# Kernel optimization log

Measured on AMD Instinct MI355X. Metric: run time of the kernel, lower is better.

Reference implementation:

```python
import jax, jax.numpy as jnp
import numpy as np


def setup_inputs() -> dict:
    key = jax.random.key(0)
    k1, k2, k3 = jax.random.split(key, 3)
    B, N, D, F = 4, 4096, 128, 128
    features = jax.random.normal(k1, (B, N, D), dtype=jnp.float32)
    A = jax.random.uniform(k2, (B, N, N), dtype=jnp.float32)
    weight = jax.random.normal(k3, (D, F), dtype=jnp.float32) * (6.0 / (D + F)) ** 0.5
    bias = jnp.zeros((F,), dtype=jnp.float32)
    return {"features": features, "A": A, "weight": weight, "bias": bias}


def reference(features, A, weight, bias):
    # aggregate: per-batch adjacency matmul  [B,N,N] @ [B,N,D] -> [B,N,D]
    agg = jnp.einsum("bnm,bmd->bnd", A, features)
    # linear transform + bias + relu  [B,N,D] @ [D,F] -> [B,N,F]
    out = jnp.einsum("bnd,df->bnf", agg, weight) + bias
    return jax.nn.relu(out)
```

## Files before the change

### kernel.cpp

```cpp
#include <hip/hip_runtime.h>
#include <hip/hip_bf16.h>

typedef __attribute__((ext_vector_type(4))) float  float4v;
typedef __attribute__((ext_vector_type(4))) short  short4v;
typedef __attribute__((ext_vector_type(8))) short  short8v;
typedef __attribute__((ext_vector_type(4))) float  f32x4;

__device__ __forceinline__ short f2bf(float f) {
  __hip_bfloat16 h = __float2bfloat16(f);
  return *reinterpret_cast<short*>(&h);
}

__device__ __forceinline__ short8v cvt8(float4v v0, float4v v1) {
  short8v s;
  s[0]=f2bf(v0[0]); s[1]=f2bf(v0[1]); s[2]=f2bf(v0[2]); s[3]=f2bf(v0[3]);
  s[4]=f2bf(v1[0]); s[5]=f2bf(v1[1]); s[6]=f2bf(v1[2]); s[7]=f2bf(v1[3]);
  return s;
}

__device__ __forceinline__ int swz(int row, int k, int ld) {
  return row * ld + (k ^ ((row & 7) << 3));
}

__device__ __forceinline__ void gll16(const void* g, void* l) {
  __builtin_amdgcn_global_load_lds(
      (const __attribute__((address_space(1))) unsigned int*)g,
      (__attribute__((address_space(3))) unsigned int*)l, 16, 0, 0);
}

__global__ __launch_bounds__(256) void k0_wt(const float* __restrict__ W,
                                             short* __restrict__ wt) {
  const int task = blockIdx.x * 256 + threadIdx.x;
  const int f = task & 127;
  const int dc = (task >> 7) * 8;
  short8v s;
#pragma unroll
  for (int j = 0; j < 8; ++j) s[j] = f2bf(W[(size_t)(dc + j) * 128 + f]);
  *(short8v*)(wt + (size_t)f * 128 + dc) = s;
}

__global__ __launch_bounds__(256) void k1_feat_x_w(
    const float* __restrict__ feat, const short* __restrict__ wt,
    short* __restrict__ ht, int N) {
  const int t = threadIdx.x;
  const int batch = blockIdx.y;
  const int m0 = blockIdx.x * 64;
  const int lane = t & 63, wid = t >> 6;
  const int lr = lane & 15, lk = (lane >> 4) * 8;
  const float* pa = feat + (size_t)batch * N * 128
                  + (size_t)(m0 + wid * 16 + lr) * 128 + lk;

  f32x4 acc[8];
#pragma unroll
  for (int j = 0; j < 8; ++j) acc[j] = (f32x4){0.f, 0.f, 0.f, 0.f};

#pragma unroll
  for (int kk = 0; kk < 4; ++kk) {
    float4v v0 = ((const float4v*)(pa + kk * 32))[0];
    float4v v1 = ((const float4v*)(pa + kk * 32))[1];
    short8v a = cvt8(v0, v1);
#pragma unroll
    for (int ni = 0; ni < 8; ++ni) {
      short8v b = *(const short8v*)(wt + (size_t)(ni * 16 + lr) * 128 + kk * 32 + lk);
      acc[ni] = __builtin_amdgcn_mfma_f32_16x16x32_bf16(a, b, acc[ni], 0, 0, 0);
    }
  }

  short* hb = ht + (size_t)batch * 128 * N;
  const int m = m0 + wid * 16 + (lane >> 4) * 4;
#pragma unroll
  for (int ni = 0; ni < 8; ++ni) {
    const int f = ni * 16 + lr;
    short4v s;
#pragma unroll
    for (int r = 0; r < 4; ++r) s[r] = f2bf(acc[ni][r]);
    *(short4v*)(hb + (size_t)f * N + m) = s;
  }
}

__global__ __launch_bounds__(256, 4) void k2_a_x_h(
    const float* __restrict__ A, const short* __restrict__ ht,
    const float* __restrict__ bias, float* __restrict__ out, int N) {
  __shared__ __align__(16) short As[2][16 * 64];
  __shared__ __align__(16) short Hs[2][128 * 64];
  const int t = threadIdx.x;

  const int nwg = gridDim.x * gridDim.y;
  int wg = blockIdx.x + gridDim.x * blockIdx.y;
  wg = (wg & 7) * (nwg >> 3) + (wg >> 3);
  const int mtiles = gridDim.x;
  const int batch = wg / mtiles;
  const int m0 = (wg - batch * mtiles) * 16;

  const float* Ab = A + (size_t)batch * N * N;
  const short* hb = ht + (size_t)batch * 128 * N;

  const int lane = t & 63, wid = t >> 6;
  const int lr = lane & 15, lk = (lane >> 4) * 8;

  const int arow = t >> 4;
  const int akc = (t & 15) * 4;

  const int hf = lane >> 3;
  const int hks = (lane & 7) * 8;

  float4v va;
  auto loadA = [&](int k0) {
    va = *(const float4v*)(Ab + (size_t)(m0 + arow) * N + k0 + akc);
  };
  auto writeA = [&](int buf) {
    short4v s;
#pragma unroll
    for (int i = 0; i < 4; ++i) s[i] = f2bf(va[i]);
    *(short4v*)(&As[buf][swz(arow, akc, 64)]) = s;
  };
  auto stageH = [&](int k0, int buf) {
#pragma unroll
    for (int i = 0; i < 4; ++i) {
      const int fb8 = (wid * 4 + i) * 8;
      const int f = fb8 + hf;
      const short* g = hb + (size_t)f * N + k0 + (hks ^ (hf << 3));
      gll16(g, &Hs[buf][fb8 * 64]);
    }
  };

  f32x4 acc[2];
  acc[0] = (f32x4){0.f, 0.f, 0.f, 0.f};
  acc[1] = (f32x4){0.f, 0.f, 0.f, 0.f};

  loadA(0);
  stageH(0, 0);
  writeA(0);
  __syncthreads();

  const int NT = N / 64;
  for (int tt = 0; tt < NT; ++tt) {
    const int cur = tt & 1;
    const bool pf = (tt + 1 < NT);
    if (pf) {
      loadA((tt + 1) * 64);
      stageH((tt + 1) * 64, cur ^ 1);
    }
#pragma unroll
    for (int kk = 0; kk < 2; ++kk) {
      const int k = kk * 32 + lk;
      short8v a = *(const short8v*)(&As[cur][swz(lr, k, 64)]);
#pragma unroll
      for (int ni = 0; ni < 2; ++ni) {
        short8v b = *(const short8v*)(&Hs[cur][swz(wid * 32 + ni * 16 + lr, k, 64)]);
        acc[ni] = __builtin_amdgcn_mfma_f32_16x16x32_bf16(a, b, acc[ni], 0, 0, 0);
      }
    }
    if (pf) writeA(cur ^ 1);
    __syncthreads();
  }

  float* ob = out + (size_t)batch * N * 128;
#pragma unroll
  for (int ni = 0; ni < 2; ++ni) {
    const int f = wid * 32 + ni * 16 + lr;
    const float bv = bias[f];
    const int mbase = m0 + (lane >> 4) * 4;
#pragma unroll
    for (int r = 0; r < 4; ++r)
      ob[(size_t)(mbase + r) * 128 + f] = fmaxf(acc[ni][r] + bv, 0.f);
  }
}

extern "C" void kernel_launch(void* const* d_in, const int* in_sizes, int n_in,
                              void* d_out, int out_size, void* d_ws, size_t ws_size,
                              hipStream_t stream) {
  const float* feat = (const float*)d_in[0];
  const float* A    = (const float*)d_in[1];
  const float* W    = (const float*)d_in[2];
  const float* bias = (const float*)d_in[3];
  float* out = (float*)d_out;

  const int featN = in_sizes[0];
  const int aN    = in_sizes[1];
  const int BN    = featN / 128;
  const int N     = aN / BN;
  const int Bb    = BN / N;

  short* wt = (short*)d_ws;
  short* ht = wt + 128 * 128;

  dim3 blk(256);
  hipLaunchKernelGGL(k0_wt, dim3(8), blk, 0, stream, W, wt);
  hipLaunchKernelGGL(k1_feat_x_w, dim3(N / 64, Bb), blk, 0, stream, feat, wt, ht, N);
  hipLaunchKernelGGL(k2_a_x_h, dim3(N / 16, Bb), blk, 0, stream, A, ht, bias, out, N);
}
```

Baseline: 93.03 us.

## Stream A directly into registers with per-wave double-buffered H and 32-row tiles

Restructures the A×H kernel so each 128-thread block handles 32 output rows. Each wave owns 64 output features and its own LDS slice of H. A is loaded straight into registers and converted to bf16 just before the MFMAs, so A no longer goes through LDS. Double buffering now uses explicit vmcnt waits instead of __syncthreads. The larger M tile halves the H re-read per output row, at the cost of far fewer waves per CU and more registers per thread.

```diff
diff --git a/kernel.cpp b/kernel.cpp
--- a/kernel.cpp
+++ b/kernel.cpp
@@ -27,6 +27,9 @@
       (const __attribute__((address_space(1))) unsigned int*)g,
       (__attribute__((address_space(3))) unsigned int*)l, 16, 0, 0);
 }
+
+#define SB() __builtin_amdgcn_sched_barrier(0)
+#define WAIT16() asm volatile("s_waitcnt vmcnt(16)" ::: "memory")
 
 __global__ __launch_bounds__(256) void k0_wt(const float* __restrict__ W,
                                              short* __restrict__ wt) {
@@ -78,92 +81,97 @@
   }
 }
 
-__global__ __launch_bounds__(256, 4) void k2_a_x_h(
+__global__ __launch_bounds__(128, 1) void k2_a_x_h(
     const float* __restrict__ A, const short* __restrict__ ht,
     const float* __restrict__ bias, float* __restrict__ out, int N) {
-  __shared__ __align__(16) short As[2][16 * 64];
-  __shared__ __align__(16) short Hs[2][128 * 64];
+  __shared__ __align__(16) short Hs[2][2][64 * 64];
   const int t = threadIdx.x;
+  const int lane = t & 63, fh = t >> 6;
 
   const int nwg = gridDim.x * gridDim.y;
   int wg = blockIdx.x + gridDim.x * blockIdx.y;
-  wg = (wg & 7) * (nwg >> 3) + (wg >> 3);
+  if ((nwg & 7) == 0) wg = (wg & 7) * (nwg >> 3) + (wg >> 3);
   const int mtiles = gridDim.x;
   const int batch = wg / mtiles;
-  const int m0 = (wg - batch * mtiles) * 16;
+  const int m0 = (wg - batch * mtiles) * 32;
 
   const float* Ab = A + (size_t)batch * N * N;
-  const short* hb = ht + (size_t)batch * 128 * N;
+  const short* hb = ht + (size_t)batch * 128 * N + (size_t)fh * 64 * N;
 
-  const int lane = t & 63, wid = t >> 6;
   const int lr = lane & 15, lk = (lane >> 4) * 8;
+  const int hf = lane >> 3, hks = (lane & 7) * 8;
 
-  const int arow = t >> 4;
-  const int akc = (t & 15) * 4;
+  short* H0 = &Hs[fh][0][0];
+  short* H1 = &Hs[fh][1][0];
 
-  const int hf = lane >> 3;
-  const int hks = (lane & 7) * 8;
-
-  float4v va;
-  auto loadA = [&](int k0) {
-    va = *(const float4v*)(Ab + (size_t)(m0 + arow) * N + k0 + akc);
-  };
-  auto writeA = [&](int buf) {
-    short4v s;
+  auto stageH = [&](int k0, short* dst) {
 #pragma unroll
-    for (int i = 0; i < 4; ++i) s[i] = f2bf(va[i]);
-    *(short4v*)(&As[buf][swz(arow, akc, 64)]) = s;
-  };
-  auto stageH = [&](int k0, int buf) {
-#pragma unroll
-    for (int i = 0; i < 4; ++i) {
-      const int fb8 = (wid * 4 + i) * 8;
-      const int f = fb8 + hf;
-      const short* g = hb + (size_t)f * N + k0 + (hks ^ (hf << 3));
-      gll16(g, &Hs[buf][fb8 * 64]);
+    for (int i = 0; i < 8; ++i) {
+      const int f8 = i * 8;
+      const short* g = hb + (size_t)(f8 + hf) * N + k0 + (hks ^ (hf << 3));
+      gll16(g, dst + f8 * 64);
     }
   };
+  auto loadA = [&](int k0, float4v (&ar)[8]) {
+    const float* p0 = Ab + (size_t)(m0 + lr) * N + k0 + lk;
+    const float* p1 = p0 + (size_t)16 * N;
+    ar[0] = ((const float4v*)p0)[0];          ar[1] = ((const float4v*)p0)[1];
+    ar[2] = ((const float4v*)(p0 + 32))[0];   ar[3] = ((const float4v*)(p0 + 32))[1];
+    ar[4] = ((const float4v*)p1)[0];          ar[5] = ((const float4v*)p1)[1];
+    ar[6] = ((const float4v*)(p1 + 32))[0];   ar[7] = ((const float4v*)(p1 + 32))[1];
+  };
 
-  f32x4 acc[2];
-  acc[0] = (f32x4){0.f, 0.f, 0.f, 0.f};
-  acc[1] = (f32x4){0.f, 0.f, 0.f, 0.f};
+  f32x4 acc[2][4];
+#pragma unroll
+  for (int i = 0; i < 2; ++i)
+#pragma unroll
+    for (int j = 0; j < 4; ++j) acc[i][j] = (f32x4){0.f, 0.f, 0.f, 0.f};
 
-  loadA(0);
-  stageH(0, 0);
-  writeA(0);
-  __syncthreads();
+  auto compute = [&](const short* Hbuf, float4v (&ar)[8]) {
+    short8v a[2][2];
+    a[0][0] = cvt8(ar[0], ar[1]);  a[0][1] = cvt8(ar[2], ar[3]);
+    a[1][0] = cvt8(ar[4], ar[5]);  a[1][1] = cvt8(ar[6], ar[7]);
+#pragma unroll
+    for (int kk = 0; kk < 2; ++kk)
+#pragma unroll
+      for (int ni = 0; ni < 4; ++ni) {
+        short8v b = *(const short8v*)(Hbuf + swz(ni * 16 + lr, kk * 32 + lk, 64));
+#pragma unroll
+        for (int mi = 0; mi < 2; ++mi)
+          acc[mi][ni] = __builtin_amdgcn_mfma_f32_16x16x32_bf16(a[mi][kk], b, acc[mi][ni], 0, 0, 0);
+      }
+  };
 
+  float4v arA[8], arB[8];
   const int NT = N / 64;
-  for (int tt = 0; tt < NT; ++tt) {
-    const int cur = tt & 1;
-    const bool pf = (tt + 1 < NT);
-    if (pf) {
-      loadA((tt + 1) * 64);
-      stageH((tt + 1) * 64, cur ^ 1);
-    }
-#pragma unroll
-    for (int kk = 0; kk < 2; ++kk) {
-      const int k = kk * 32 + lk;
-      short8v a = *(const short8v*)(&As[cur][swz(lr, k, 64)]);
-#pragma unroll
-      for (int ni = 0; ni < 2; ++ni) {
-        short8v b = *(const short8v*)(&Hs[cur][swz(wid * 32 + ni * 16 + lr, k, 64)]);
-        acc[ni] = __builtin_amdgcn_mfma_f32_16x16x32_bf16(a, b, acc[ni], 0, 0, 0);
-      }
-    }
-    if (pf) writeA(cur ^ 1);
-    __syncthreads();
+
+  stageH(0, H0);
+  loadA(0, arA);
+  for (int tt = 0; tt < NT; tt += 2) {
+    const int kn = (tt + 1) * 64;
+    stageH(kn, H1);
+    loadA(kn, arB);
+    SB(); WAIT16(); SB();
+    compute(H0, arA);
+    const int kn2 = (tt + 2 < NT) ? (tt + 2) * 64 : (NT - 1) * 64;
+    stageH(kn2, H0);
+    loadA(kn2, arA);
+    SB(); WAIT16(); SB();
+    compute(H1, arB);
   }
 
-  float* ob = out + (size_t)batch * N * 128;
+  float* ob = out + (size_t)batch * N * 128 + fh * 64;
 #pragma unroll
-  for (int ni = 0; ni < 2; ++ni) {
-    const int f = wid * 32 + ni * 16 + lr;
-    const float bv = bias[f];
-    const int mbase = m0 + (lane >> 4) * 4;
+  for (int ni = 0; ni < 4; ++ni) {
+    const int fl = ni * 16 + lr;
+    const float bv = bias[fh * 64 + fl];
 #pragma unroll
-    for (int r = 0; r < 4; ++r)
-      ob[(size_t)(mbase + r) * 128 + f] = fmaxf(acc[ni][r] + bv, 0.f);
+    for (int mi = 0; mi < 2; ++mi) {
+      const int mbase = m0 + mi * 16 + (lane >> 4) * 4;
+#pragma unroll
+      for (int r = 0; r < 4; ++r)
+        ob[(size_t)(mbase + r) * 128 + fl] = fmaxf(acc[mi][ni][r] + bv, 0.f);
+    }
   }
 }
 
@@ -185,8 +193,7 @@
   short* wt = (short*)d_ws;
   short* ht = wt + 128 * 128;
 
-  dim3 blk(256);
-  hipLaunchKernelGGL(k0_wt, dim3(8), blk, 0, stream, W, wt);
-  hipLaunchKernelGGL(k1_feat_x_w, dim3(N / 64, Bb), blk, 0, stream, feat, wt, ht, N);
-  hipLaunchKernelGGL(k2_a_x_h, dim3(N / 16, Bb), blk, 0, stream, A, ht, bias, out, N);
+  hipLaunchKernelGGL(k0_wt, dim3(8), dim3(256), 0, stream, W, wt);
+  hipLaunchKernelGGL(k1_feat_x_w, dim3(N / 64, Bb), dim3(256), 0, stream, feat, wt, ht, N);
+  hipLaunchKernelGGL(k2_a_x_h, dim3(N / 32, Bb), dim3(128), 0, stream, A, ht, bias, out, N);
 }
```

Result: slower. 105.7 us (+13.6%).

## Enlarge k2 row tile to 64 with direct-register A loads and triple-buffered H

Applied to the files above, without the earlier changes.

The A×H kernel now gives each block 64 output rows instead of 16. Each wave holds a 16x128 accumulator and loads its A fragment straight from global memory into registers, with no LDS staging. The H tile is triple-buffered through global_load_lds, and the pipeline uses explicit vmcnt waits with one barrier per step, so each H tile is reused by four times as many rows. The cost is a grid four times smaller (1024 blocks), higher register pressure and reliance on hand-tuned vmcnt counts that assume a particular load ordering.

```diff
diff --git a/kernel.cpp b/kernel.cpp
--- a/kernel.cpp
+++ b/kernel.cpp
@@ -78,89 +78,94 @@
   }
 }
 
-__global__ __launch_bounds__(256, 4) void k2_a_x_h(
+__global__ __launch_bounds__(256, 1) void k2_a_x_h(
     const float* __restrict__ A, const short* __restrict__ ht,
     const float* __restrict__ bias, float* __restrict__ out, int N) {
-  __shared__ __align__(16) short As[2][16 * 64];
-  __shared__ __align__(16) short Hs[2][128 * 64];
+  __shared__ __align__(16) short Hs[3][128 * 64];
   const int t = threadIdx.x;
+  const int lane = t & 63, wid = t >> 6;
 
   const int nwg = gridDim.x * gridDim.y;
   int wg = blockIdx.x + gridDim.x * blockIdx.y;
-  wg = (wg & 7) * (nwg >> 3) + (wg >> 3);
+  if ((nwg & 7) == 0) wg = (wg & 7) * (nwg >> 3) + (wg >> 3);
   const int mtiles = gridDim.x;
   const int batch = wg / mtiles;
-  const int m0 = (wg - batch * mtiles) * 16;
+  const int m0 = (wg - batch * mtiles) * 64;
 
   const float* Ab = A + (size_t)batch * N * N;
   const short* hb = ht + (size_t)batch * 128 * N;
 
-  const int lane = t & 63, wid = t >> 6;
   const int lr = lane & 15, lk = (lane >> 4) * 8;
+  const int hf = lane >> 3, hks = (lane & 7) * 8;
 
-  const int arow = t >> 4;
-  const int akc = (t & 15) * 4;
+  const float* pa = Ab + (size_t)(m0 + wid * 16 + lr) * N + lk;
 
-  const int hf = lane >> 3;
-  const int hks = (lane & 7) * 8;
-
-  float4v va;
-  auto loadA = [&](int k0) {
-    va = *(const float4v*)(Ab + (size_t)(m0 + arow) * N + k0 + akc);
-  };
-  auto writeA = [&](int buf) {
-    short4v s;
-#pragma unroll
-    for (int i = 0; i < 4; ++i) s[i] = f2bf(va[i]);
-    *(short4v*)(&As[buf][swz(arow, akc, 64)]) = s;
-  };
-  auto stageH = [&](int k0, int buf) {
+  auto stageH = [&](int k0, short* dst) {
 #pragma unroll
     for (int i = 0; i < 4; ++i) {
-      const int fb8 = (wid * 4 + i) * 8;
-      const int f = fb8 + hf;
-      const short* g = hb + (size_t)f * N + k0 + (hks ^ (hf << 3));
-      gll16(g, &Hs[buf][fb8 * 64]);
+      const int f8 = (wid * 4 + i) * 8;
+      const short* g = hb + (size_t)(f8 + hf) * N + k0 + (hks ^ (hf << 3));
+      gll16(g, dst + f8 * 64);
+    }
+  };
+  auto loadA = [&](int k0, float4v (&ar)[4]) {
+    const float* p = pa + k0;
+    ar[0] = ((const float4v*)p)[0];
+    ar[1] = ((const float4v*)p)[1];
+    ar[2] = ((const float4v*)(p + 32))[0];
+    ar[3] = ((const float4v*)(p + 32))[1];
+  };
+
+  f32x4 acc[8];
+#pragma unroll
+  for (int j = 0; j < 8; ++j) acc[j] = (f32x4){0.f, 0.f, 0.f, 0.f};
+
+  auto compute = [&](const short* Hbuf, float4v (&ar)[4]) {
+    short8v a0 = cvt8(ar[0], ar[1]);
+    short8v a1 = cvt8(ar[2], ar[3]);
+#pragma unroll
+    for (int ni = 0; ni < 8; ++ni) {
+      short8v b = *(const short8v*)(Hbuf + swz(ni * 16 + lr, lk, 64));
+      acc[ni] = __builtin_amdgcn_mfma_f32_16x16x32_bf16(a0, b, acc[ni], 0, 0, 0);
+    }
+#pragma unroll
+    for (int ni = 0; ni < 8; ++ni) {
+      short8v b = *(const short8v*)(Hbuf + swz(ni * 16 + lr, 32 + lk, 64));
+      acc[ni] = __builtin_amdgcn_mfma_f32_16x16x32_bf16(a1, b, acc[ni], 0, 0, 0);
     }
   };
 
-  f32x4 acc[2];
-  acc[0] = (f32x4){0.f, 0.f, 0.f, 0.f};
-  acc[1] = (f32x4){0.f, 0.f, 0.f, 0.f};
+  float4v arE[4], arO[4];
+  const int NT = N / 64;
 
-  loadA(0);
-  stageH(0, 0);
-  writeA(0);
-  __syncthreads();
+  stageH(0, &Hs[0][0]);
+  loadA(0, arE);
+  stageH(64, &Hs[1][0]);
+  loadA(64, arO);
 
-  const int NT = N / 64;
-  for (int tt = 0; tt < NT; ++tt) {
-    const int cur = tt & 1;
-    const bool pf = (tt + 1 < NT);
-    if (pf) {
-      loadA((tt + 1) * 64);
-      stageH((tt + 1) * 64, cur ^ 1);
-    }
-#pragma unroll
-    for (int kk = 0; kk < 2; ++kk) {
-      const int k = kk * 32 + lk;
-      short8v a = *(const short8v*)(&As[cur][swz(lr, k, 64)]);
-#pragma unroll
-      for (int ni = 0; ni < 2; ++ni) {
-        short8v b = *(const short8v*)(&Hs[cur][swz(wid * 32 + ni * 16 + lr, k, 64)]);
-        acc[ni] = __builtin_amdgcn_mfma_f32_16x16x32_bf16(a, b, acc[ni], 0, 0, 0);
-      }
-    }
-    if (pf) writeA(cur ^ 1);
-    __syncthreads();
+#define K2_BODY(T_, AR_)                                                     \
+  {                                                                          \
+    const int t_ = (T_);                                                     \
+    if (t_ == NT - 1) { asm volatile("s_waitcnt vmcnt(4)" ::: "memory"); }   \
+    else              { asm volatile("s_waitcnt vmcnt(12)" ::: "memory"); }  \
+    __builtin_amdgcn_s_barrier();                                            \
+    if (t_ + 2 < NT) stageH((t_ + 2) * 64, &Hs[(t_ + 2) % 3][0]);            \
+    compute(&Hs[t_ % 3][0], AR_);                                            \
+    if (t_ + 2 < NT) loadA((t_ + 2) * 64, AR_);                              \
   }
+
+  for (int tt = 0; tt < NT; tt += 2) {
+    K2_BODY(tt, arE);
+    K2_BODY(tt + 1, arO);
+  }
+#undef K2_BODY
 
   float* ob = out + (size_t)batch * N * 128;
 #pragma unroll
-  for (int ni = 0; ni < 2; ++ni) {
-    const int f = wid * 32 + ni * 16 + lr;
+  for (int ni = 0; ni < 8; ++ni) {
+    const int f = ni * 16 + lr;
     const float bv = bias[f];
-    const int mbase = m0 + (lane >> 4) * 4;
+    const int mbase = m0 + wid * 16 + (lane >> 4) * 4;
 #pragma unroll
     for (int r = 0; r < 4; ++r)
       ob[(size_t)(mbase + r) * 128 + f] = fmaxf(acc[ni][r] + bv, 0.f);
@@ -185,8 +190,7 @@
   short* wt = (short*)d_ws;
   short* ht = wt + 128 * 128;
 
-  dim3 blk(256);
-  hipLaunchKernelGGL(k0_wt, dim3(8), blk, 0, stream, W, wt);
-  hipLaunchKernelGGL(k1_feat_x_w, dim3(N / 64, Bb), blk, 0, stream, feat, wt, ht, N);
-  hipLaunchKernelGGL(k2_a_x_h, dim3(N / 16, Bb), blk, 0, stream, A, ht, bias, out, N);
+  hipLaunchKernelGGL(k0_wt, dim3(8), dim3(256), 0, stream, W, wt);
+  hipLaunchKernelGGL(k1_feat_x_w, dim3(N / 64, Bb), dim3(256), 0, stream, feat, wt, ht, N);
+  hipLaunchKernelGGL(k2_a_x_h, dim3(N / 64, Bb), dim3(256), 0, stream, A, ht, bias, out, N);
 }
```

Measured after the change: 91.68 us. Within noise of the previous version (-1.4%).

## Split-K the adjacency GEMM with 32-row tiles and stage H transpose through LDS

Applied to the files above, without the earlier changes.

The A×H kernel now uses 32-row M tiles, so each staged H tile is reused across twice as many rows. It can optionally split K in two, writing fp32 partials that a new combine kernel sums before adding bias and ReLU. The feat×W kernel now transposes its output through shared memory so global stores are coalesced 16-byte rows. Split-K keeps the grid size constant despite larger tiles, but it adds an extra partials write and read of B*N*128 floats twice, plus another launch, and needs a larger workspace.

```diff
diff --git a/kernel.cpp b/kernel.cpp
--- a/kernel.cpp
+++ b/kernel.cpp
@@ -42,6 +42,7 @@
 __global__ __launch_bounds__(256) void k1_feat_x_w(
     const float* __restrict__ feat, const short* __restrict__ wt,
     short* __restrict__ ht, int N) {
+  __shared__ short T[128][72];
   const int t = threadIdx.x;
   const int batch = blockIdx.y;
   const int m0 = blockIdx.x * 64;
@@ -66,22 +67,32 @@
     }
   }
 
+  const int mloc = wid * 16 + (lane >> 4) * 4;
+#pragma unroll
+  for (int ni = 0; ni < 8; ++ni) {
+    short4v s;
+#pragma unroll
+    for (int r = 0; r < 4; ++r) s[r] = f2bf(acc[ni][r]);
+    *(short4v*)(&T[ni * 16 + lr][mloc]) = s;
+  }
+  __syncthreads();
+
   short* hb = ht + (size_t)batch * 128 * N;
-  const int m = m0 + wid * 16 + (lane >> 4) * 4;
-#pragma unroll
-  for (int ni = 0; ni < 8; ++ni) {
-    const int f = ni * 16 + lr;
-    short4v s;
-#pragma unroll
-    for (int r = 0; r < 4; ++r) s[r] = f2bf(acc[ni][r]);
-    *(short4v*)(hb + (size_t)f * N + m) = s;
-  }
-}
-
+#pragma unroll
+  for (int it = 0; it < 4; ++it) {
+    const int idx = it * 256 + t;
+    const int f = idx >> 3;
+    const int mc = (idx & 7) * 8;
+    short8v v = *(const short8v*)(&T[f][mc]);
+    *(short8v*)(hb + (size_t)f * N + m0 + mc) = v;
+  }
+}
+
+template<int NSPLIT>
 __global__ __launch_bounds__(256, 4) void k2_a_x_h(
     const float* __restrict__ A, const short* __restrict__ ht,
-    const float* __restrict__ bias, float* __restrict__ out, int N) {
-  __shared__ __align__(16) short As[2][16 * 64];
+    const float* __restrict__ bias, float* __restrict__ dst, int N) {
+  __shared__ __align__(16) short As[2][32 * 64];
   __shared__ __align__(16) short Hs[2][128 * 64];
   const int t = threadIdx.x;
 
@@ -89,30 +100,33 @@
   int wg = blockIdx.x + gridDim.x * blockIdx.y;
   wg = (wg & 7) * (nwg >> 3) + (wg >> 3);
   const int mtiles = gridDim.x;
-  const int batch = wg / mtiles;
-  const int m0 = (wg - batch * mtiles) * 16;
+  const int combo = wg / mtiles;
+  const int kh = (NSPLIT == 2) ? (combo & 1) : 0;
+  const int batch = (NSPLIT == 2) ? (combo >> 1) : combo;
+  const int m0 = (wg - combo * mtiles) * 32;
+  const int kbase = kh * (N / NSPLIT);
 
   const float* Ab = A + (size_t)batch * N * N;
   const short* hb = ht + (size_t)batch * 128 * N;
 
   const int lane = t & 63, wid = t >> 6;
+  const int mi = wid >> 1, fj = wid & 1;
   const int lr = lane & 15, lk = (lane >> 4) * 8;
 
-  const int arow = t >> 4;
-  const int akc = (t & 15) * 4;
+  const int arow = t >> 3;
+  const int akc = (t & 7) * 8;
 
   const int hf = lane >> 3;
   const int hks = (lane & 7) * 8;
 
-  float4v va;
+  float4v va0, va1;
   auto loadA = [&](int k0) {
-    va = *(const float4v*)(Ab + (size_t)(m0 + arow) * N + k0 + akc);
+    const float* p = Ab + (size_t)(m0 + arow) * N + k0 + akc;
+    va0 = ((const float4v*)p)[0];
+    va1 = ((const float4v*)p)[1];
   };
   auto writeA = [&](int buf) {
-    short4v s;
-#pragma unroll
-    for (int i = 0; i < 4; ++i) s[i] = f2bf(va[i]);
-    *(short4v*)(&As[buf][swz(arow, akc, 64)]) = s;
+    *(short8v*)(&As[buf][swz(arow, akc, 64)]) = cvt8(va0, va1);
   };
   auto stageH = [&](int k0, int buf) {
 #pragma unroll
@@ -124,30 +138,30 @@
     }
   };
 
-  f32x4 acc[2];
-  acc[0] = (f32x4){0.f, 0.f, 0.f, 0.f};
-  acc[1] = (f32x4){0.f, 0.f, 0.f, 0.f};
-
-  loadA(0);
-  stageH(0, 0);
+  f32x4 acc[4];
+#pragma unroll
+  for (int j = 0; j < 4; ++j) acc[j] = (f32x4){0.f, 0.f, 0.f, 0.f};
+
+  loadA(kbase);
+  stageH(kbase, 0);
   writeA(0);
   __syncthreads();
 
-  const int NT = N / 64;
+  const int NT = (N / NSPLIT) / 64;
   for (int tt = 0; tt < NT; ++tt) {
     const int cur = tt & 1;
     const bool pf = (tt + 1 < NT);
     if (pf) {
-      loadA((tt + 1) * 64);
-      stageH((tt + 1) * 64, cur ^ 1);
+      loadA(kbase + (tt + 1) * 64);
+      stageH(kbase + (tt + 1) * 64, cur ^ 1);
     }
 #pragma unroll
     for (int kk = 0; kk < 2; ++kk) {
       const int k = kk * 32 + lk;
-      short8v a = *(const short8v*)(&As[cur][swz(lr, k, 64)]);
-#pragma unroll
-      for (int ni = 0; ni < 2; ++ni) {
-        short8v b = *(const short8v*)(&Hs[cur][swz(wid * 32 + ni * 16 + lr, k, 64)]);
+      short8v a = *(const short8v*)(&As[cur][swz(mi * 16 + lr, k, 64)]);
+#pragma unroll
+      for (int ni = 0; ni < 4; ++ni) {
+        short8v b = *(const short8v*)(&Hs[cur][swz(fj * 64 + ni * 16 + lr, k, 64)]);
         acc[ni] = __builtin_amdgcn_mfma_f32_16x16x32_bf16(a, b, acc[ni], 0, 0, 0);
       }
     }
@@ -155,15 +169,42 @@
     __syncthreads();
   }
 
-  float* ob = out + (size_t)batch * N * 128;
-#pragma unroll
-  for (int ni = 0; ni < 2; ++ni) {
-    const int f = wid * 32 + ni * 16 + lr;
-    const float bv = bias[f];
-    const int mbase = m0 + (lane >> 4) * 4;
-#pragma unroll
-    for (int r = 0; r < 4; ++r)
-      ob[(size_t)(mbase + r) * 128 + f] = fmaxf(acc[ni][r] + bv, 0.f);
+  if (NSPLIT == 2) {
+    float* pb = dst + ((size_t)kh * gridDim.y / 2 * mtiles * 32 + (size_t)batch * N) * 128;
+#pragma unroll
+    for (int ni = 0; ni < 4; ++ni) {
+      const int f = fj * 64 + ni * 16 + lr;
+      const int mbase = m0 + mi * 16 + (lane >> 4) * 4;
+#pragma unroll
+      for (int r = 0; r < 4; ++r)
+        pb[(size_t)(mbase + r) * 128 + f] = acc[ni][r];
+    }
+  } else {
+    float* ob = dst + (size_t)batch * N * 128;
+#pragma unroll
+    for (int ni = 0; ni < 4; ++ni) {
+      const int f = fj * 64 + ni * 16 + lr;
+      const float bv = bias[f];
+      const int mbase = m0 + mi * 16 + (lane >> 4) * 4;
+#pragma unroll
+      for (int r = 0; r < 4; ++r)
+        ob[(size_t)(mbase + r) * 128 + f] = fmaxf(acc[ni][r] + bv, 0.f);
+    }
+  }
+}
+
+__global__ __launch_bounds__(256) void k3_combine(
+    const float* __restrict__ p0, const float* __restrict__ p1,
+    const float* __restrict__ bias, float* __restrict__ out, long total4) {
+  const long stride = (long)gridDim.x * 256;
+  for (long i = blockIdx.x * 256L + threadIdx.x; i < total4; i += stride) {
+    float4v a = ((const float4v*)p0)[i];
+    float4v b = ((const float4v*)p1)[i];
+    float4v bv = ((const float4v*)bias)[i & 31];
+    float4v o;
+#pragma unroll
+    for (int j = 0; j < 4; ++j) o[j] = fmaxf(a[j] + b[j] + bv[j], 0.f);
+    ((float4v*)out)[i] = o;
   }
 }
 
@@ -184,9 +225,22 @@
 
   short* wt = (short*)d_ws;
   short* ht = wt + 128 * 128;
-
-  dim3 blk(256);
-  hipLaunchKernelGGL(k0_wt, dim3(8), blk, 0, stream, W, wt);
-  hipLaunchKernelGGL(k1_feat_x_w, dim3(N / 64, Bb), blk, 0, stream, feat, wt, ht, N);
-  hipLaunchKernelGGL(k2_a_x_h, dim3(N / 16, Bb), blk, 0, stream, A, ht, bias, out, N);
-}
+  float* part = (float*)(ht + (size_t)Bb * 128 * N);
+
+  const size_t need = 128 * 128 * 2 + (size_t)Bb * 128 * N * 2
+                    + (size_t)2 * Bb * N * 128 * 4;
+
+  hipLaunchKernelGGL(k0_wt, dim3(8), dim3(256), 0, stream, W, wt);
+  hipLaunchKernelGGL(k1_feat_x_w, dim3(N / 64, Bb), dim3(256), 0, stream, feat, wt, ht, N);
+
+  if (ws_size >= need && (N / 32) % 1 == 0) {
+    hipLaunchKernelGGL((k2_a_x_h<2>), dim3(N / 32, 2 * Bb), dim3(256), 0, stream,
+                       A, ht, bias, part, N);
+    const long total4 = (long)Bb * N * 32;
+    hipLaunchKernelGGL(k3_combine, dim3(2048), dim3(256), 0, stream,
+                       part, part + (size_t)Bb * N * 128, bias, out, total4);
+  } else {
+    hipLaunchKernelGGL((k2_a_x_h<1>), dim3(N / 32, Bb), dim3(256), 0, stream,
+                       A, ht, bias, out, N);
+  }
+}
```

After: 95.63 us. +2.8%, slower.
